# Kernel optimization log

Measured on AMD Instinct MI355X. Metric: run time of the kernel, lower is better.

The kernel has to match this reference:

```python
import jax, jax.numpy as jnp
import numpy as np

S, B, T, D = 25, 64, 640, 128
NUM_CHANNELS = 4
T_WAV = 1.0 / 16000.0
LOG_F_MEAN = 5.02654
LOG_F_STD = 0.373288


def _i_2pi():
    # harmonic index per output dim: dims grouped as num_freq blocks of num_channels
    i = jnp.floor_divide(jnp.arange(D), NUM_CHANNELS) + 1  # [D]
    return i.astype(jnp.float32) * (2.0 * np.pi)


def _k_T():
    return jnp.arange(T, dtype=jnp.float32) * T_WAV  # [T]


def setup_inputs() -> dict:
    key = jax.random.key(0)
    k1, k2, k3, k4, k5 = jax.random.split(key, 5)
    x = jax.random.normal(k1, (S, B, 1, T), dtype=jnp.float32)
    nlf = jax.random.normal(k2, (S, B, 1, 1), dtype=jnp.float32)
    tau = jax.random.uniform(k3, (S, B, 1, 1), dtype=jnp.float32)
    a = 0.1 + 0.1 * jax.random.normal(k4, (D,), dtype=jnp.float32)
    phi = jax.random.normal(k5, (D,), dtype=jnp.float32)
    return {"x": x, "nlf": nlf, "tau": tau, "a": a, "phi": phi}


def reference(x, nlf, tau, a, phi):
    i_2pi = _i_2pi()          # [D]
    k_T = _k_T()              # [T]
    f = jnp.exp(nlf[..., 0, 0] * LOG_F_STD + LOG_F_MEAN)   # [S,B]
    t = k_T[None, None, :] - tau[..., 0, :]                  # [S,B,T]
    f_t = f[..., None] * t                                   # [S,B,T]
    # deg: [S,B,T,D] = f_t outer i_2pi + phi ; sin basis
    deg = f_t[..., None] * i_2pi[None, None, None, :] + phi
    s = jnp.sin(deg)                                         # [S,B,T,D]
    x_SBT = x[:, :, 0, :]                                    # [S,B,T]
    sin_x = jnp.einsum('sbtd,sbt->sbd', s, x_SBT)            # [S,B,D]
    h = a * sin_x                                            # [S,B,D]
    return h
```

## Files before the change

kernel.cpp:

```cpp
#include <hip/hip_runtime.h>
#include <math.h>


#define S_DIM 25
#define B_DIM 64
#define T_DIM 640
#define D_DIM 128
#define NCHUNK 8
#define CLEN (T_DIM / NCHUNK)

__global__ __launch_bounds__(256) void sinenet_kernel(
    const float* __restrict__ x,
    const float* __restrict__ nlf,
    const float* __restrict__ tau,
    const float* __restrict__ a,
    const float* __restrict__ phi,
    float* __restrict__ out)
{
    __shared__ float lds_x[T_DIM];
    __shared__ float red[2][NCHUNK][32];
    __shared__ float fin[64];

    const int bid   = blockIdx.x;
    const int tid   = threadIdx.x;
    const int lane  = tid & 63;
    const int wid   = tid >> 6;
    const int h     = lane & 31;
    const int chunk = wid * 2 + (lane >> 5);
    const int t0    = chunk * CLEN;

    for (int t = tid; t < T_DIM; t += 256)
        lds_x[t] = x[(size_t)bid * T_DIM + t];

    const float tau_v = tau[bid];
    const float f     = expf(nlf[bid] * 0.373288f + 5.02654f);
    const float i_f   = (float)(h + 1);
    const float T_WAV = 1.0f / 16000.0f;

    const float dr0 = i_f * (f * T_WAV);
    const float dr  = dr0 - floorf(dr0);
    const float sD  = __builtin_amdgcn_sinf(dr);
    const float cD  = __builtin_amdgcn_cosf(dr);

    const float tv0 = (float)t0 * T_WAV - tau_v;
    const float ft0 = f * tv0;
    const float u0  = ft0 - floorf(ft0);
    const float p0  = i_f * u0;
    const float w0  = p0 - floorf(p0);
    float s = __builtin_amdgcn_sinf(w0);
    float c = __builtin_amdgcn_cosf(w0);

    __syncthreads();

    float acc_s = 0.0f, acc_c = 0.0f;
    const float* __restrict__ xp = &lds_x[t0];
    #pragma unroll 8
    for (int t = 0; t < CLEN; ++t) {
        const float xt = xp[t];
        acc_s = fmaf(xt, s, acc_s);
        acc_c = fmaf(xt, c, acc_c);
        const float s2 = fmaf(s, cD, c * sD);
        const float c2 = fmaf(c, cD, -(s * sD));
        s = s2; c = c2;
    }

    red[0][chunk][h] = acc_s;
    red[1][chunk][h] = acc_c;
    __syncthreads();

    if (tid < 64) {
        const int part = tid >> 5, hh = tid & 31;
        float v = 0.0f;
        #pragma unroll
        for (int cc = 0; cc < NCHUNK; ++cc)
            v += red[part][cc][hh];
        fin[tid] = v;
    }
    __syncthreads();

    if (tid < D_DIM) {
        const int   i0 = tid >> 2;
        const float Ss = fin[i0];
        const float Cs = fin[32 + i0];
        const float ph = phi[tid];
        out[(size_t)bid * D_DIM + tid] = a[tid] * fmaf(cosf(ph), Ss, sinf(ph) * Cs);
    }
}

extern "C" void kernel_launch(void* const* d_in, const int* in_sizes, int n_in,
                              void* d_out, int out_size, void* d_ws, size_t ws_size,
                              hipStream_t stream) {
    const float* x   = (const float*)d_in[0];
    const float* nlf = (const float*)d_in[1];
    const float* tau = (const float*)d_in[2];
    const float* a   = (const float*)d_in[3];
    const float* phi = (const float*)d_in[4];
    float* out = (float*)d_out;

    const int n_sb = S_DIM * B_DIM;
    sinenet_kernel<<<n_sb, 256, 0, stream>>>(x, nlf, tau, a, phi, out);
}
```

Before: 11.38 us.

## Block the rotation recurrence by 8 steps with precomputed rotation powers

The serial sin/cos rotation recurrence in the inner loop is restructured into 8-step blocks. Rotation powers c1..c8/s1..s8 are precomputed, each block's x samples are folded into two dot products P and Q, and the phasor advances once per block. This shortens the dependent FMA chain and reduces rotation work per sample. The change also vectorises the LDS load and the reads of x with float4, and swaps libm sinf/cosf on phi for hardware sin/cos after range reduction, which may slightly change accuracy.

After: 9.474 us, median of 2. 16.7% less time.

```diff
diff --git a/kernel.cpp b/kernel.cpp
--- a/kernel.cpp
+++ b/kernel.cpp
@@ -29,8 +29,9 @@
     const int chunk = wid * 2 + (lane >> 5);
     const int t0    = chunk * CLEN;
 
-    for (int t = tid; t < T_DIM; t += 256)
-        lds_x[t] = x[(size_t)bid * T_DIM + t];
+    if (tid < T_DIM / 4)
+        reinterpret_cast<float4*>(lds_x)[tid] =
+            reinterpret_cast<const float4*>(x + (size_t)bid * T_DIM)[tid];
 
     const float tau_v = tau[bid];
     const float f     = expf(nlf[bid] * 0.373288f + 5.02654f);
@@ -41,6 +42,15 @@
     const float dr  = dr0 - floorf(dr0);
     const float sD  = __builtin_amdgcn_sinf(dr);
     const float cD  = __builtin_amdgcn_cosf(dr);
+
+    const float c1 = cD,                        s1 = sD;
+    const float c2 = fmaf(c1, cD, -(s1 * sD)),  s2 = fmaf(s1, cD, c1 * sD);
+    const float c3 = fmaf(c2, cD, -(s2 * sD)),  s3 = fmaf(s2, cD, c2 * sD);
+    const float c4 = fmaf(c3, cD, -(s3 * sD)),  s4 = fmaf(s3, cD, c3 * sD);
+    const float c5 = fmaf(c4, cD, -(s4 * sD)),  s5 = fmaf(s4, cD, c4 * sD);
+    const float c6 = fmaf(c5, cD, -(s5 * sD)),  s6 = fmaf(s5, cD, c5 * sD);
+    const float c7 = fmaf(c6, cD, -(s6 * sD)),  s7 = fmaf(s6, cD, c6 * sD);
+    const float c8 = fmaf(c7, cD, -(s7 * sD)),  s8 = fmaf(s7, cD, c7 * sD);
 
     const float tv0 = (float)t0 * T_WAV - tau_v;
     const float ft0 = f * tv0;
@@ -53,15 +63,27 @@
     __syncthreads();
 
     float acc_s = 0.0f, acc_c = 0.0f;
-    const float* __restrict__ xp = &lds_x[t0];
-    #pragma unroll 8
-    for (int t = 0; t < CLEN; ++t) {
-        const float xt = xp[t];
-        acc_s = fmaf(xt, s, acc_s);
-        acc_c = fmaf(xt, c, acc_c);
-        const float s2 = fmaf(s, cD, c * sD);
-        const float c2 = fmaf(c, cD, -(s * sD));
-        s = s2; c = c2;
+    const float4* __restrict__ xp4 = reinterpret_cast<const float4*>(&lds_x[t0]);
+    #pragma unroll
+    for (int m = 0; m < CLEN / 8; ++m) {
+        const float4 xa = xp4[2 * m];
+        const float4 xb = xp4[2 * m + 1];
+
+        float P = xa.x;
+        P = fmaf(xa.y, c1, P); P = fmaf(xa.z, c2, P); P = fmaf(xa.w, c3, P);
+        P = fmaf(xb.x, c4, P); P = fmaf(xb.y, c5, P); P = fmaf(xb.z, c6, P);
+        P = fmaf(xb.w, c7, P);
+
+        float Q = xa.y * s1;
+        Q = fmaf(xa.z, s2, Q); Q = fmaf(xa.w, s3, Q); Q = fmaf(xb.x, s4, Q);
+        Q = fmaf(xb.y, s5, Q); Q = fmaf(xb.z, s6, Q); Q = fmaf(xb.w, s7, Q);
+
+        acc_s = fmaf(s, P, acc_s); acc_s = fmaf(c, Q, acc_s);
+        acc_c = fmaf(c, P, acc_c); acc_c = fmaf(-s, Q, acc_c);
+
+        const float sn = fmaf(s, c8, c * s8);
+        const float cn = fmaf(c, c8, -(s * s8));
+        s = sn; c = cn;
     }
 
     red[0][chunk][h] = acc_s;
@@ -82,8 +104,11 @@
         const int   i0 = tid >> 2;
         const float Ss = fin[i0];
         const float Cs = fin[32 + i0];
-        const float ph = phi[tid];
-        out[(size_t)bid * D_DIM + tid] = a[tid] * fmaf(cosf(ph), Ss, sinf(ph) * Cs);
+        float pr = phi[tid] * 0.15915494309189535f;
+        pr = pr - floorf(pr);
+        const float sp = __builtin_amdgcn_sinf(pr);
+        const float cp = __builtin_amdgcn_cosf(pr);
+        out[(size_t)bid * D_DIM + tid] = a[tid] * fmaf(cp, Ss, sp * Cs);
     }
 }
 
```
